# Performance work log

Hardware: AMD Instinct MI355X
Metric: run time of the kernel (lower is better)

The kernel has to match this reference:

```python
import jax, jax.numpy as jnp
import numpy as np

RES = 0.16      # config.resolution (m)
XMIN = -51.2    # config.x_min
YMIN = -51.2    # config.y_min
EPS = 1e-5      # BatchNorm eps
NEG = -1.0e9


def setup_inputs() -> dict:
    key = jax.random.key(0)
    ks = jax.random.split(key, 12)
    P, M = 100000, 32
    C_IN, C_MID, C_OUT = 9, 64, 64
    pillars = jax.random.normal(ks[0], (P, M, 4), dtype=jnp.float32)
    pillar_coords = jax.random.randint(ks[1], (P, 2), 0, 640, dtype=jnp.int64)
    num_points_per_pillar = jax.random.randint(ks[2], (P,), 0, 33, dtype=jnp.int64)
    # MLP params (Linear stored as (in,out) for x @ W + b)
    W1 = jax.random.normal(ks[3], (C_IN, C_MID), dtype=jnp.float32) / np.sqrt(C_IN)
    b1 = jax.random.normal(ks[4], (C_MID,), dtype=jnp.float32) * 0.01
    g1 = jnp.ones((C_MID,), jnp.float32)
    beta1 = jnp.zeros((C_MID,), jnp.float32)
    m1 = jax.random.normal(ks[5], (C_MID,), dtype=jnp.float32) * 0.1
    v1 = jax.random.uniform(ks[6], (C_MID,), dtype=jnp.float32, minval=0.5, maxval=1.5)
    W2 = jax.random.normal(ks[7], (C_MID, C_OUT), dtype=jnp.float32) / np.sqrt(C_MID)
    b2 = jax.random.normal(ks[8], (C_OUT,), dtype=jnp.float32) * 0.01
    g2 = jnp.ones((C_OUT,), jnp.float32)
    beta2 = jnp.zeros((C_OUT,), jnp.float32)
    m2 = jax.random.normal(ks[9], (C_OUT,), dtype=jnp.float32) * 0.1
    v2 = jax.random.uniform(ks[10], (C_OUT,), dtype=jnp.float32, minval=0.5, maxval=1.5)
    return {
        "pillars": pillars, "pillar_coords": pillar_coords,
        "num_points_per_pillar": num_points_per_pillar,
        "W1": W1, "b1": b1, "g1": g1, "beta1": beta1, "m1": m1, "v1": v1,
        "W2": W2, "b2": b2, "g2": g2, "beta2": beta2, "m2": m2, "v2": v2,
    }


def reference(pillars, pillar_coords, num_points_per_pillar,
              W1, b1, g1, beta1, m1, v1, W2, b2, g2, beta2, m2, v2):
    P, M, _ = pillars.shape
    # pillar centers from grid indices
    xc = (pillar_coords[:, 1].astype(jnp.float32) + 0.5) * RES + XMIN  # (P,)
    yc = (pillar_coords[:, 0].astype(jnp.float32) + 0.5) * RES + YMIN  # (P,)
    npts = num_points_per_pillar.astype(jnp.float32)
    mask = (jnp.arange(M)[None, :] < num_points_per_pillar[:, None]).astype(pillars.dtype)  # (P,M)
    x, y, z, r = pillars[:, :, 0], pillars[:, :, 1], pillars[:, :, 2], pillars[:, :, 3]
    z_mean = (z * mask).sum(axis=1) / jnp.clip(npts, 1.0)  # (P,)
    xo = x - xc[:, None]
    yo = y - yc[:, None]
    zo = z - z_mean[:, None]
    feat = jnp.stack([x, y, z, r, xo, yo, zo, xo, yo], axis=-1)  # (P,M,9)
    # shared MLP: Linear -> BN(eval) -> ReLU, twice
    h = feat @ W1 + b1
    h = jax.nn.relu(g1 * (h - m1) * jax.lax.rsqrt(v1 + EPS) + beta1)
    h = h @ W2 + b2
    h = jax.nn.relu(g2 * (h - m2) * jax.lax.rsqrt(v2 + EPS) + beta2)  # (P,M,64)
    # masked max over points per pillar
    m3 = mask[:, :, None]
    h = h * m3 + (1.0 - m3) * NEG
    return h.max(axis=1)  # (P,64)
```

## Files before the change

### kernel.cpp

```cpp
#include <hip/hip_runtime.h>
#include <type_traits>

#define RES_ 0.16f
#define XMIN_ -51.2f
#define YMIN_ -51.2f
#define EPS_ 1e-5f
#define NEG_ -1000000000.0f

#define WPB 4

typedef _Float16 f16x8 __attribute__((ext_vector_type(8)));
typedef _Float16 f16x4 __attribute__((ext_vector_type(4)));
typedef _Float16 f16x2 __attribute__((ext_vector_type(2)));
typedef float f32x4 __attribute__((ext_vector_type(4)));

union F8u { f16x8 v; f16x2 h[4]; };
union F4u { f16x4 v; f16x2 h[2]; };

static __device__ __forceinline__ f16x2 pkrtz(float a, float b) {
    return __builtin_bit_cast(f16x2, __builtin_amdgcn_cvt_pkrtz(a, b));
}

static __device__ __forceinline__ f16x2 relu2(f16x2 x) {
#if __has_builtin(__builtin_elementwise_max)
    const f16x2 z2 = (f16x2)(_Float16)0.f;
    return __builtin_elementwise_max(x, z2);
#else
    f16x2 r;
    r[0] = x[0] > (_Float16)0.f ? x[0] : (_Float16)0.f;
    r[1] = x[1] > (_Float16)0.f ? x[1] : (_Float16)0.f;
    return r;
#endif
}

static __device__ __forceinline__ float fast_rcp(float x) {
#if __has_builtin(__builtin_amdgcn_rcpf)
    return __builtin_amdgcn_rcpf(x);
#else
    return 1.0f / x;
#endif
}

template <int CTRL>
static __device__ __forceinline__ float dpp_ror_add(float x) {
    int r = __builtin_amdgcn_update_dpp(0, __float_as_int(x), CTRL, 0xf, 0xf, true);
    return x + __int_as_float(r);
}

static __device__ __forceinline__ float xmax16(float x) {
    float a = x, b = x;
    asm("v_permlane16_swap_b32 %0, %1" : "+v"(a), "+v"(b));
    return fmaxf(a, b);
}
static __device__ __forceinline__ float xmax32(float x) {
    float a = x, b = x;
    asm("v_permlane32_swap_b32 %0, %1" : "+v"(a), "+v"(b));
    return fmaxf(a, b);
}

__global__ __launch_bounds__(256, 4) void pfn_kernel(
    const float* __restrict__ pillars,
    const int* __restrict__ coords,
    const int* __restrict__ npts_arr,
    const float* __restrict__ W1, const float* __restrict__ b1,
    const float* __restrict__ g1, const float* __restrict__ beta1,
    const float* __restrict__ m1, const float* __restrict__ v1,
    const float* __restrict__ W2, const float* __restrict__ b2,
    const float* __restrict__ g2, const float* __restrict__ beta2,
    const float* __restrict__ m2, const float* __restrict__ v2,
    float* __restrict__ out, int P)
{
    const int tid  = threadIdx.x;
    const int wave = tid >> 6;
    const int lane = tid & 63;
    const int quad = lane >> 4;
    const int col  = lane & 15;

    f16x4 aw1[4];
#pragma unroll
    for (int mt = 0; mt < 4; ++mt) {
        const int ch = mt * 16 + col;
        const float a1 = g1[ch] * rsqrtf(v1[ch] + EPS_);
        const float c1 = fmaf(a1, b1[ch] - m1[ch], beta1[ch]);
#pragma unroll
        for (int j = 0; j < 4; ++j) {
            const int k = quad * 4 + j;
            float w;
            if (k < 9)        w = a1 * W1[k * 64 + ch];
            else if (k == 9)  w = c1;
            else if (k == 10) w = a1 * W1[6 * 64 + ch];
            else              w = 0.0f;
            aw1[mt][j] = (_Float16)w;
        }
    }

    f16x8 bw2[2][4];
#pragma unroll
    for (int nt = 0; nt < 4; ++nt) {
        const int n0 = nt * 16 + col;
        const float a2 = g2[n0] * rsqrtf(v2[n0] + EPS_);
#pragma unroll
        for (int kt = 0; kt < 2; ++kt)
#pragma unroll
            for (int j = 0; j < 8; ++j) {
                const int c = 32 * kt + 16 * (j >> 2) + 4 * quad + (j & 3);
                bw2[kt][nt][j] = (_Float16)(a2 * W2[c * 64 + n0]);
            }
    }
    const float c2own = fmaf(g2[lane] * rsqrtf(v2[lane] + EPS_),
                             b2[lane] - m2[lane], beta2[lane]);

    auto zreduce = [&](const float4& A, const float4& B, int n) -> float {
        float zs = (col < n) ? A.z : 0.0f;
        zs += (16 + col < n) ? B.z : 0.0f;
        zs = dpp_ror_add<0x128>(zs);
        zs = dpp_ror_add<0x124>(zs);
        zs = dpp_ror_add<0x122>(zs);
        zs = dpp_ror_add<0x121>(zs);
        return zs * fast_rcp(fmaxf((float)n, 1.0f));
    };

    const int nwaves = gridDim.x * WPB;
    int p = __builtin_amdgcn_readfirstlane(blockIdx.x * WPB + wave);
    if (p >= P) return;

    const float4* pb = (const float4*)(pillars + (size_t)p * 128);
    float4 ptA = pb[col];
    float4 ptB = pb[16 + col];
    int np = npts_arr[p];
    int cy = coords[2 * p], cx = coords[2 * p + 1];
    np = np < 0 ? 0 : (np > 32 ? 32 : np);
    float z_cur = zreduce(ptA, ptB, np);

    while (true) {
        const int pn = p + nwaves;
        const bool has_next = pn < P;
        float4 ptAn, ptBn; int npn = 0, cyn = 0, cxn = 0;
        if (has_next) {
            const float4* pbn = (const float4*)(pillars + (size_t)pn * 128);
            ptAn = pbn[col];
            ptBn = pbn[16 + col];
            npn = npts_arr[pn];
            cyn = coords[2 * pn]; cxn = coords[2 * pn + 1];
        }

        const int npu = __builtin_amdgcn_readfirstlane(np);
        const float xc = ((float)cx + 0.5f) * RES_ + XMIN_;
        const float yc = ((float)cy + 0.5f) * RES_ + YMIN_;
        const float z_mean = z_cur;

        auto body = [&](auto MTC) -> float {
            constexpr int MT = decltype(MTC)::value;
            float hm4[4] = {NEG_, NEG_, NEG_, NEG_};

#pragma unroll
            for (int t = 0; t < MT; ++t) {
                const float4 pt = (t == 0) ? ptA : ptB;

                const float xo = pt.x - xc;
                const float yo = pt.y - yc;
                const f16x2 c01 = pkrtz(pt.x, pt.y);
                const f16x2 c23 = pkrtz(pt.z, pt.w);
                const f16x2 c45 = pkrtz(xo, yo);
                const f16x2 c67 = pkrtz(pt.z, xo);
                const f16x2 c89 = pkrtz(yo, 1.0f);
                const f16x2 cab = pkrtz(-z_mean, 0.0f);
                const f16x2 z2  = (f16x2)(_Float16)0.f;
                F4u u;
                u.h[0] = (quad == 0) ? c01 : (quad == 1) ? c45 : (quad == 2) ? c89 : z2;
                u.h[1] = (quad == 0) ? c23 : (quad == 1) ? c67 : (quad == 2) ? cab : z2;
                const f16x4 bt = u.v;

                f32x4 acc1[4];
                const f32x4 zz = {0.f, 0.f, 0.f, 0.f};
#pragma unroll
                for (int mt = 0; mt < 4; ++mt)
                    acc1[mt] = __builtin_amdgcn_mfma_f32_16x16x16f16(aw1[mt], bt, zz, 0, 0, 0);

                f16x8 av2[2];
#pragma unroll
                for (int kt = 0; kt < 2; ++kt) {
                    F8u w;
                    w.h[0] = relu2(pkrtz(acc1[2 * kt][0],     acc1[2 * kt][1]));
                    w.h[1] = relu2(pkrtz(acc1[2 * kt][2],     acc1[2 * kt][3]));
                    w.h[2] = relu2(pkrtz(acc1[2 * kt + 1][0], acc1[2 * kt + 1][1]));
                    w.h[3] = relu2(pkrtz(acc1[2 * kt + 1][2], acc1[2 * kt + 1][3]));
                    av2[kt] = w.v;
                }

                f32x4 cm;
#pragma unroll
                for (int r = 0; r < 4; ++r)
                    cm[r] = (t * 16 + quad * 4 + r < np) ? 0.0f : NEG_;

#pragma unroll
                for (int nt = 0; nt < 4; ++nt) {
                    f32x4 acc = __builtin_amdgcn_mfma_f32_16x16x32_f16(av2[0], bw2[0][nt], cm, 0, 0, 0);
                    acc = __builtin_amdgcn_mfma_f32_16x16x32_f16(av2[1], bw2[1][nt], acc, 0, 0, 0);
                    hm4[nt] = fmaxf(fmaxf(hm4[nt], fmaxf(acc[0], acc[1])),
                                    fmaxf(acc[2], acc[3]));
                }
            }

            float hmv[4];
#pragma unroll
            for (int nt = 0; nt < 4; ++nt)
                hmv[nt] = xmax32(xmax16(hm4[nt]));
            float r0 = (quad == 0) ? hmv[0] : (quad == 1) ? hmv[1] : (quad == 2) ? hmv[2] : hmv[3];
            return fmaxf(r0 + c2own, 0.0f);
        };

        float res;
        if (npu > 16)     res = body(std::integral_constant<int, 2>{});
        else if (npu > 0) res = body(std::integral_constant<int, 1>{});
        else              res = NEG_;
        out[(size_t)p * 64 + lane] = res;

        if (!has_next) break;

        npn = npn < 0 ? 0 : (npn > 32 ? 32 : npn);
        z_cur = zreduce(ptAn, ptBn, npn);

        p = pn; ptA = ptAn; ptB = ptBn; np = npn; cy = cyn; cx = cxn;
    }
}

extern "C" void kernel_launch(void* const* d_in, const int* in_sizes, int n_in,
                              void* d_out, int out_size, void* d_ws, size_t ws_size,
                              hipStream_t stream) {
    const float* pillars = (const float*)d_in[0];
    const int*   coords  = (const int*)d_in[1];
    const int*   npts    = (const int*)d_in[2];
    const float* W1      = (const float*)d_in[3];
    const float* b1      = (const float*)d_in[4];
    const float* g1      = (const float*)d_in[5];
    const float* beta1   = (const float*)d_in[6];
    const float* m1      = (const float*)d_in[7];
    const float* v1      = (const float*)d_in[8];
    const float* W2      = (const float*)d_in[9];
    const float* b2      = (const float*)d_in[10];
    const float* g2      = (const float*)d_in[11];
    const float* beta2   = (const float*)d_in[12];
    const float* m2      = (const float*)d_in[13];
    const float* v2      = (const float*)d_in[14];
    float* out           = (float*)d_out;

    const int P = in_sizes[2];
    const int blocks = 1024;

    hipLaunchKernelGGL(pfn_kernel, dim3(blocks), dim3(256), 0, stream,
                       pillars, coords, npts, W1, b1, g1, beta1, m1, v1,
                       W2, b2, g2, beta2, m2, v2, out, P);
}
```

Measured before the change: 151.4 us.

## Process two pillars per wave iteration to interleave independent MFMA chains

Each wave now handles a pair of pillars per loop iteration. It interleaves the MFMA chains, repacking and max reductions of the two pillars so independent work can hide MFMA latency, and it prefetches both next pillars. The loop trip count is set by the larger point count of the pair, so some work is wasted when the counts differ. Launch bounds drop to 3 blocks per CU to give room for the extra registers, which lowers occupancy.

```diff
diff --git a/kernel.cpp b/kernel.cpp
--- a/kernel.cpp
+++ b/kernel.cpp
@@ -58,7 +58,7 @@
     return fmaxf(a, b);
 }
 
-__global__ __launch_bounds__(256, 4) void pfn_kernel(
+__global__ __launch_bounds__(256, 3) void pfn_kernel(
     const float* __restrict__ pillars,
     const int* __restrict__ coords,
     const int* __restrict__ npts_arr,
@@ -120,108 +120,157 @@
         return zs * fast_rcp(fmaxf((float)n, 1.0f));
     };
 
-    const int nwaves = gridDim.x * WPB;
-    int p = __builtin_amdgcn_readfirstlane(blockIdx.x * WPB + wave);
-    if (p >= P) return;
-
-    const float4* pb = (const float4*)(pillars + (size_t)p * 128);
-    float4 ptA = pb[col];
-    float4 ptB = pb[16 + col];
-    int np = npts_arr[p];
-    int cy = coords[2 * p], cx = coords[2 * p + 1];
-    np = np < 0 ? 0 : (np > 32 ? 32 : np);
-    float z_cur = zreduce(ptA, ptB, np);
+    const int nw = gridDim.x * WPB;
+    const int npairs = (P + 1) >> 1;
+    int pr = __builtin_amdgcn_readfirstlane(blockIdx.x * WPB + wave);
+    if (pr >= npairs) return;
+
+    int p0 = pr * 2;
+    {
+    }
+    const float4* pb0 = (const float4*)(pillars + (size_t)p0 * 128);
+    const int p1c = (p0 + 1 < P) ? p0 + 1 : P - 1;
+    const float4* pb1 = (const float4*)(pillars + (size_t)p1c * 128);
+    float4 ptA0 = pb0[col],      ptB0 = pb0[16 + col];
+    float4 ptA1 = pb1[col],      ptB1 = pb1[16 + col];
+    int np0 = npts_arr[p0];
+    int np1 = (p0 + 1 < P) ? npts_arr[p0 + 1] : 0;
+    int cy0 = coords[2 * p0],  cx0 = coords[2 * p0 + 1];
+    int cy1 = coords[2 * p1c], cx1 = coords[2 * p1c + 1];
+    np0 = np0 < 0 ? 0 : (np0 > 32 ? 32 : np0);
+    np1 = np1 < 0 ? 0 : (np1 > 32 ? 32 : np1);
+    float z0 = zreduce(ptA0, ptB0, np0);
+    float z1 = zreduce(ptA1, ptB1, np1);
 
     while (true) {
-        const int pn = p + nwaves;
-        const bool has_next = pn < P;
-        float4 ptAn, ptBn; int npn = 0, cyn = 0, cxn = 0;
+        const int prn = pr + nw;
+        const bool has_next = prn < npairs;
+        float4 nA0, nB0, nA1, nB1;
+        int nnp0 = 0, nnp1 = 0, ncy0 = 0, ncx0 = 0, ncy1 = 0, ncx1 = 0;
         if (has_next) {
-            const float4* pbn = (const float4*)(pillars + (size_t)pn * 128);
-            ptAn = pbn[col];
-            ptBn = pbn[16 + col];
-            npn = npts_arr[pn];
-            cyn = coords[2 * pn]; cxn = coords[2 * pn + 1];
+            const int q0 = prn * 2;
+            const int q1c = (q0 + 1 < P) ? q0 + 1 : P - 1;
+            const float4* qb0 = (const float4*)(pillars + (size_t)q0 * 128);
+            const float4* qb1 = (const float4*)(pillars + (size_t)q1c * 128);
+            nA0 = qb0[col];  nB0 = qb0[16 + col];
+            nA1 = qb1[col];  nB1 = qb1[16 + col];
+            nnp0 = npts_arr[q0];
+            nnp1 = (q0 + 1 < P) ? npts_arr[q0 + 1] : 0;
+            ncy0 = coords[2 * q0];  ncx0 = coords[2 * q0 + 1];
+            ncy1 = coords[2 * q1c]; ncx1 = coords[2 * q1c + 1];
         }
 
-        const int npu = __builtin_amdgcn_readfirstlane(np);
-        const float xc = ((float)cx + 0.5f) * RES_ + XMIN_;
-        const float yc = ((float)cy + 0.5f) * RES_ + YMIN_;
-        const float z_mean = z_cur;
-
-        auto body = [&](auto MTC) -> float {
+        const int u0 = __builtin_amdgcn_readfirstlane(np0);
+        const int u1 = __builtin_amdgcn_readfirstlane(np1);
+        const int um = u0 > u1 ? u0 : u1;
+        const float xc0f = ((float)cx0 + 0.5f) * RES_ + XMIN_;
+        const float yc0f = ((float)cy0 + 0.5f) * RES_ + YMIN_;
+        const float xc1f = ((float)cx1 + 0.5f) * RES_ + XMIN_;
+        const float yc1f = ((float)cy1 + 0.5f) * RES_ + YMIN_;
+        const float zm0 = z0, zm1 = z1;
+
+        auto packB = [&](const float4& pt, float xcv, float ycv, float zmv) -> f16x4 {
+            const float xo = pt.x - xcv;
+            const float yo = pt.y - ycv;
+            const f16x2 c01 = pkrtz(pt.x, pt.y);
+            const f16x2 c23 = pkrtz(pt.z, pt.w);
+            const f16x2 c45 = pkrtz(xo, yo);
+            const f16x2 c67 = pkrtz(pt.z, xo);
+            const f16x2 c89 = pkrtz(yo, 1.0f);
+            const f16x2 cab = pkrtz(-zmv, 0.0f);
+            const f16x2 z2  = (f16x2)(_Float16)0.f;
+            F4u u;
+            u.h[0] = (quad == 0) ? c01 : (quad == 1) ? c45 : (quad == 2) ? c89 : z2;
+            u.h[1] = (quad == 0) ? c23 : (quad == 1) ? c67 : (quad == 2) ? cab : z2;
+            return u.v;
+        };
+        auto repack = [&](const f32x4* a, f16x8* v) {
+#pragma unroll
+            for (int kt = 0; kt < 2; ++kt) {
+                F8u w;
+                w.h[0] = relu2(pkrtz(a[2 * kt][0],     a[2 * kt][1]));
+                w.h[1] = relu2(pkrtz(a[2 * kt][2],     a[2 * kt][3]));
+                w.h[2] = relu2(pkrtz(a[2 * kt + 1][0], a[2 * kt + 1][1]));
+                w.h[3] = relu2(pkrtz(a[2 * kt + 1][2], a[2 * kt + 1][3]));
+                v[kt] = w.v;
+            }
+        };
+
+        float res0 = NEG_, res1 = NEG_;
+
+        auto body2 = [&](auto MTC) {
             constexpr int MT = decltype(MTC)::value;
-            float hm4[4] = {NEG_, NEG_, NEG_, NEG_};
+            float h0[4] = {NEG_, NEG_, NEG_, NEG_};
+            float h1[4] = {NEG_, NEG_, NEG_, NEG_};
 
 #pragma unroll
             for (int t = 0; t < MT; ++t) {
-                const float4 pt = (t == 0) ? ptA : ptB;
-
-                const float xo = pt.x - xc;
-                const float yo = pt.y - yc;
-                const f16x2 c01 = pkrtz(pt.x, pt.y);
-                const f16x2 c23 = pkrtz(pt.z, pt.w);
-                const f16x2 c45 = pkrtz(xo, yo);
-                const f16x2 c67 = pkrtz(pt.z, xo);
-                const f16x2 c89 = pkrtz(yo, 1.0f);
-                const f16x2 cab = pkrtz(-z_mean, 0.0f);
-                const f16x2 z2  = (f16x2)(_Float16)0.f;
-                F4u u;
-                u.h[0] = (quad == 0) ? c01 : (quad == 1) ? c45 : (quad == 2) ? c89 : z2;
-                u.h[1] = (quad == 0) ? c23 : (quad == 1) ? c67 : (quad == 2) ? cab : z2;
-                const f16x4 bt = u.v;
-
-                f32x4 acc1[4];
+                const float4 q0 = (t == 0) ? ptA0 : ptB0;
+                const float4 q1 = (t == 0) ? ptA1 : ptB1;
+                const f16x4 bt0 = packB(q0, xc0f, yc0f, zm0);
+                const f16x4 bt1 = packB(q1, xc1f, yc1f, zm1);
+
+                f32x4 a0[4], a1[4];
                 const f32x4 zz = {0.f, 0.f, 0.f, 0.f};
 #pragma unroll
-                for (int mt = 0; mt < 4; ++mt)
-                    acc1[mt] = __builtin_amdgcn_mfma_f32_16x16x16f16(aw1[mt], bt, zz, 0, 0, 0);
-
-                f16x8 av2[2];
-#pragma unroll
-                for (int kt = 0; kt < 2; ++kt) {
-                    F8u w;
-                    w.h[0] = relu2(pkrtz(acc1[2 * kt][0],     acc1[2 * kt][1]));
-                    w.h[1] = relu2(pkrtz(acc1[2 * kt][2],     acc1[2 * kt][3]));
-                    w.h[2] = relu2(pkrtz(acc1[2 * kt + 1][0], acc1[2 * kt + 1][1]));
-                    w.h[3] = relu2(pkrtz(acc1[2 * kt + 1][2], acc1[2 * kt + 1][3]));
-                    av2[kt] = w.v;
+                for (int mt = 0; mt < 4; ++mt) {
+                    a0[mt] = __builtin_amdgcn_mfma_f32_16x16x16f16(aw1[mt], bt0, zz, 0, 0, 0);
+                    a1[mt] = __builtin_amdgcn_mfma_f32_16x16x16f16(aw1[mt], bt1, zz, 0, 0, 0);
                 }
 
-                f32x4 cm;
-#pragma unroll
-                for (int r = 0; r < 4; ++r)
-                    cm[r] = (t * 16 + quad * 4 + r < np) ? 0.0f : NEG_;
+                f16x8 v0[2], v1[2];
+                repack(a0, v0);
+                repack(a1, v1);
+
+                f32x4 cm0, cm1;
+#pragma unroll
+                for (int r = 0; r < 4; ++r) {
+                    const int row = t * 16 + quad * 4 + r;
+                    cm0[r] = (row < np0) ? 0.0f : NEG_;
+                    cm1[r] = (row < np1) ? 0.0f : NEG_;
+                }
 
 #pragma unroll
                 for (int nt = 0; nt < 4; ++nt) {
-                    f32x4 acc = __builtin_amdgcn_mfma_f32_16x16x32_f16(av2[0], bw2[0][nt], cm, 0, 0, 0);
-                    acc = __builtin_amdgcn_mfma_f32_16x16x32_f16(av2[1], bw2[1][nt], acc, 0, 0, 0);
-                    hm4[nt] = fmaxf(fmaxf(hm4[nt], fmaxf(acc[0], acc[1])),
-                                    fmaxf(acc[2], acc[3]));
+                    f32x4 x0 = __builtin_amdgcn_mfma_f32_16x16x32_f16(v0[0], bw2[0][nt], cm0, 0, 0, 0);
+                    f32x4 x1 = __builtin_amdgcn_mfma_f32_16x16x32_f16(v1[0], bw2[0][nt], cm1, 0, 0, 0);
+                    x0 = __builtin_amdgcn_mfma_f32_16x16x32_f16(v0[1], bw2[1][nt], x0, 0, 0, 0);
+                    x1 = __builtin_amdgcn_mfma_f32_16x16x32_f16(v1[1], bw2[1][nt], x1, 0, 0, 0);
+                    h0[nt] = fmaxf(fmaxf(h0[nt], fmaxf(x0[0], x0[1])), fmaxf(x0[2], x0[3]));
+                    h1[nt] = fmaxf(fmaxf(h1[nt], fmaxf(x1[0], x1[1])), fmaxf(x1[2], x1[3]));
                 }
             }
 
-            float hmv[4];
-#pragma unroll
-            for (int nt = 0; nt < 4; ++nt)
-                hmv[nt] = xmax32(xmax16(hm4[nt]));
-            float r0 = (quad == 0) ? hmv[0] : (quad == 1) ? hmv[1] : (quad == 2) ? hmv[2] : hmv[3];
-            return fmaxf(r0 + c2own, 0.0f);
+            float e0[4], e1[4];
+#pragma unroll
+            for (int nt = 0; nt < 4; ++nt) {
+                e0[nt] = xmax32(xmax16(h0[nt]));
+                e1[nt] = xmax32(xmax16(h1[nt]));
+            }
+            const float s0 = (quad == 0) ? e0[0] : (quad == 1) ? e0[1] : (quad == 2) ? e0[2] : e0[3];
+            const float s1 = (quad == 0) ? e1[0] : (quad == 1) ? e1[1] : (quad == 2) ? e1[2] : e1[3];
+            res0 = fmaxf(s0 + c2own, 0.0f);
+            res1 = fmaxf(s1 + c2own, 0.0f);
         };
 
-        float res;
-        if (npu > 16)     res = body(std::integral_constant<int, 2>{});
-        else if (npu > 0) res = body(std::integral_constant<int, 1>{});
-        else              res = NEG_;
-        out[(size_t)p * 64 + lane] = res;
+        if (um > 16)     body2(std::integral_constant<int, 2>{});
+        else if (um > 0) body2(std::integral_constant<int, 1>{});
+
+        out[(size_t)p0 * 64 + lane] = (u0 > 0) ? res0 : NEG_;
+        if (p0 + 1 < P)
+            out[(size_t)(p0 + 1) * 64 + lane] = (u1 > 0) ? res1 : NEG_;
 
         if (!has_next) break;
 
-        npn = npn < 0 ? 0 : (npn > 32 ? 32 : npn);
-        z_cur = zreduce(ptAn, ptBn, npn);
-
-        p = pn; ptA = ptAn; ptB = ptBn; np = npn; cy = cyn; cx = cxn;
+        nnp0 = nnp0 < 0 ? 0 : (nnp0 > 32 ? 32 : nnp0);
+        nnp1 = nnp1 < 0 ? 0 : (nnp1 > 32 ? 32 : nnp1);
+        z0 = zreduce(nA0, nB0, nnp0);
+        z1 = zreduce(nA1, nB1, nnp1);
+
+        pr = prn; p0 = prn * 2;
+        ptA0 = nA0; ptB0 = nB0; ptA1 = nA1; ptB1 = nB1;
+        np0 = nnp0; np1 = nnp1;
+        cy0 = ncy0; cx0 = ncx0; cy1 = ncy1; cx1 = ncx1;
     }
 }
 
```

Result: slower. 167.1 us (+10.4%).

## Move layer-2 weights from registers to LDS and raise occupancy

Applied to the files above, without the earlier changes.

The second-layer weight fragments (32 f16x8 registers per lane) now live in shared memory, built cooperatively once per block. Each tile reads them back with paired ds_read_b128 followed by an immediate wait. This frees VGPRs so launch bounds can request 5 waves per SIMD, and the grid grows to 1280 blocks to match. The trade-off is eight LDS reads per pillar tile, each pair stalling on lgkmcnt(0) before its MFMA, which adds latency to the inner loop.

```diff
diff --git a/kernel.cpp b/kernel.cpp
--- a/kernel.cpp
+++ b/kernel.cpp
@@ -58,7 +58,16 @@
     return fmaxf(a, b);
 }
 
-__global__ __launch_bounds__(256, 4) void pfn_kernel(
+template <int IDX0, int IDX1>
+static __device__ __forceinline__ void lds_read2_b128(unsigned base, f16x8& a, f16x8& b) {
+    asm volatile("ds_read_b128 %0, %2 offset:%c3\n\t"
+                 "ds_read_b128 %1, %2 offset:%c4\n\t"
+                 "s_waitcnt lgkmcnt(0)"
+                 : "=v"(a), "=v"(b)
+                 : "v"(base), "i"(IDX0 * 1024), "i"(IDX1 * 1024));
+}
+
+__global__ __launch_bounds__(256, 5) void pfn_kernel(
     const float* __restrict__ pillars,
     const int* __restrict__ coords,
     const int* __restrict__ npts_arr,
@@ -76,6 +85,24 @@
     const int quad = lane >> 4;
     const int col  = lane & 15;
 
+    __shared__ _Float16 bw2s[8][64][8];
+
+    {
+        const int nt = wave;
+        const int n0 = nt * 16 + col;
+        const float a2 = g2[n0] * rsqrtf(v2[n0] + EPS_);
+#pragma unroll
+        for (int kt = 0; kt < 2; ++kt) {
+            F8u w;
+#pragma unroll
+            for (int j = 0; j < 8; ++j) {
+                const int c = 32 * kt + 16 * (j >> 2) + 4 * quad + (j & 3);
+                w.v[j] = (_Float16)(a2 * W2[c * 64 + n0]);
+            }
+            *(f16x8*)&bw2s[kt * 4 + nt][lane][0] = w.v;
+        }
+    }
+
     f16x4 aw1[4];
 #pragma unroll
     for (int mt = 0; mt < 4; ++mt) {
@@ -93,22 +120,12 @@
             aw1[mt][j] = (_Float16)w;
         }
     }
-
-    f16x8 bw2[2][4];
-#pragma unroll
-    for (int nt = 0; nt < 4; ++nt) {
-        const int n0 = nt * 16 + col;
-        const float a2 = g2[n0] * rsqrtf(v2[n0] + EPS_);
-#pragma unroll
-        for (int kt = 0; kt < 2; ++kt)
-#pragma unroll
-            for (int j = 0; j < 8; ++j) {
-                const int c = 32 * kt + 16 * (j >> 2) + 4 * quad + (j & 3);
-                bw2[kt][nt][j] = (_Float16)(a2 * W2[c * 64 + n0]);
-            }
-    }
     const float c2own = fmaf(g2[lane] * rsqrtf(v2[lane] + EPS_),
                              b2[lane] - m2[lane], beta2[lane]);
+
+    __syncthreads();
+
+    const unsigned bwbase = (unsigned)(size_t)&bw2s[0][lane][0];
 
     auto zreduce = [&](const float4& A, const float4& B, int n) -> float {
         float zs = (col < n) ? A.z : 0.0f;
@@ -193,13 +210,19 @@
                 for (int r = 0; r < 4; ++r)
                     cm[r] = (t * 16 + quad * 4 + r < np) ? 0.0f : NEG_;
 
-#pragma unroll
-                for (int nt = 0; nt < 4; ++nt) {
-                    f32x4 acc = __builtin_amdgcn_mfma_f32_16x16x32_f16(av2[0], bw2[0][nt], cm, 0, 0, 0);
-                    acc = __builtin_amdgcn_mfma_f32_16x16x32_f16(av2[1], bw2[1][nt], acc, 0, 0, 0);
+                auto nts = [&](auto NTC) {
+                    constexpr int nt = decltype(NTC)::value;
+                    f16x8 b0, b1;
+                    lds_read2_b128<nt, 4 + nt>(bwbase, b0, b1);
+                    f32x4 acc = __builtin_amdgcn_mfma_f32_16x16x32_f16(av2[0], b0, cm, 0, 0, 0);
+                    acc = __builtin_amdgcn_mfma_f32_16x16x32_f16(av2[1], b1, acc, 0, 0, 0);
                     hm4[nt] = fmaxf(fmaxf(hm4[nt], fmaxf(acc[0], acc[1])),
                                     fmaxf(acc[2], acc[3]));
-                }
+                };
+                nts(std::integral_constant<int, 0>{});
+                nts(std::integral_constant<int, 1>{});
+                nts(std::integral_constant<int, 2>{});
+                nts(std::integral_constant<int, 3>{});
             }
 
             float hmv[4];
@@ -246,7 +269,7 @@
     float* out           = (float*)d_out;
 
     const int P = in_sizes[2];
-    const int blocks = 1024;
+    const int blocks = 1280;
 
     hipLaunchKernelGGL(pfn_kernel, dim3(blocks), dim3(256), 0, stream,
                        pillars, coords, npts, W1, b1, g1, beta1, m1, v1,
```

New measurement: 154.3 us. Within noise of the previous version (+2.0%).
